# Optimization experiments

Measured on AMD Instinct MI355X. Metric: run time of the kernel, lower is better.

The kernel has to match this reference:

```python
import jax, jax.numpy as jnp
from jax import lax
import numpy as np

B, T, C, H = 2048, 1024, 9, 36  # batch, seq_len, input_size, hidden_size


def setup_inputs() -> dict:
    key = jax.random.key(0)
    ks = jax.random.split(key, 4)
    x = jax.random.normal(ks[0], (B, T, C), dtype=jnp.float32)
    # torch GRU param shapes: weight_ih (3H, C), weight_hh (3H, H), biases (3H,)
    w_ih = jax.random.normal(ks[1], (3 * H, C), dtype=jnp.float32) * (1.0 / np.sqrt(C))
    w_hh = jax.random.normal(ks[2], (3 * H, H), dtype=jnp.float32) * (1.0 / np.sqrt(H))
    b_ih = jnp.zeros((3 * H,), dtype=jnp.float32)
    b_hh = jnp.zeros((3 * H,), dtype=jnp.float32)
    w_head = jax.random.normal(ks[3], (1, H), dtype=jnp.float32) * (1.0 / np.sqrt(H))
    b_head = jnp.zeros((1,), dtype=jnp.float32)
    return {"x": x, "w_ih": w_ih, "w_hh": w_hh, "b_ih": b_ih, "b_hh": b_hh,
            "w_head": w_head, "b_head": b_head}


def reference(x, w_ih, w_hh, b_ih, b_hh, w_head, b_head):
    """TinyGRUInt8.forward in fp32 (Quant/DeQuant stubs are identity).
    GRU (batch_first, torch gate order r,z,n), take last timestep, Linear head.
    """
    h = w_hh.shape[1]
    # Precompute input contribution to all gates for every timestep: (B,T,3H)
    gx = jnp.einsum('btc,gc->btg', x, w_ih) + b_ih
    gx = jnp.moveaxis(gx, 1, 0)  # (T,B,3H) for scan over time

    def step(h_prev, gxt):
        gh = h_prev @ w_hh.T + b_hh                      # (B,3H)
        r = jax.nn.sigmoid(gxt[:, :h] + gh[:, :h])
        z = jax.nn.sigmoid(gxt[:, h:2 * h] + gh[:, h:2 * h])
        n = jnp.tanh(gxt[:, 2 * h:] + r * gh[:, 2 * h:])
        h_new = (1.0 - z) * n + z * h_prev
        return h_new, None

    h0 = jnp.zeros((x.shape[0], h), dtype=x.dtype)
    h_last, _ = lax.scan(step, h0, gx)                   # last output == final hidden
    return h_last @ w_head.T + b_head                    # (B,1)
```

## Files before the change

kernel.cpp:

```cpp
#include <hip/hip_runtime.h>

typedef float     v2f __attribute__((ext_vector_type(2)));
typedef _Float16  v2h __attribute__((ext_vector_type(2)));
typedef unsigned int uint;

#define BB 2048
#define TT 1024
#define CC 9
#define HH 36
#define G3 108
#define CSTEPS 64
#define CF (CSTEPS * CC)
#define XP 12
#define NCH (TT / CSTEPS)

__device__ __forceinline__ void lds_fence() {
    asm volatile("" ::: "memory");
    __builtin_amdgcn_sched_barrier(0);
}

__device__ __forceinline__ void pinh(v2h& v) {
    uint t = __builtin_bit_cast(uint, v);
    asm volatile("" : "+v"(t));
    v = __builtin_bit_cast(v2h, t);
}
__device__ __forceinline__ void pin2f(v2f& v) {
    uint64_t t = __builtin_bit_cast(uint64_t, v);
    asm volatile("" : "+v"(t));
    v = __builtin_bit_cast(v2f, t);
}

__device__ __forceinline__ void gload4(const float* g, float* l) {
    __builtin_amdgcn_global_load_lds(
        (const __attribute__((address_space(1))) unsigned int*)g,
        (__attribute__((address_space(3))) unsigned int*)l,
        4, 0, 0);
}

__global__ __launch_bounds__(64)
__attribute__((amdgpu_waves_per_eu(2, 2)))
void gru_kernel(
    const float* __restrict__ x,
    const float* __restrict__ w_ih,
    const float* __restrict__ w_hh,
    const float* __restrict__ b_ih,
    const float* __restrict__ b_hh,
    const float* __restrict__ w_head,
    const float* __restrict__ b_head,
    float* __restrict__ out)
{
    const int b = blockIdx.x;
    const int l = threadIdx.x;

    __shared__ __align__(16) float    fstage[CF];
    __shared__ __align__(16) float    xpad[CSTEPS * XP];
    __shared__ __align__(16) float    pbuf[256];
    __shared__ __align__(16) _Float16 hbuf[40];

    const int i0 = (2 * l     < G3) ? 2 * l     : G3 - 1;
    const int i1 = (2 * l + 1 < G3) ? 2 * l + 1 : G3 - 1;

    v2h wh0[18], wh1[18];
    v2f wx0[4], wx1[4];
    float w80, w81;
    float bA0, bB0, bA1, bB1;
    {
        const float* p0 = w_hh + (size_t)i0 * HH;
        const float* p1 = w_hh + (size_t)i1 * HH;
#pragma unroll
        for (int k = 0; k < 18; ++k) {
            wh0[k] = (v2h){(_Float16)p0[2*k], (_Float16)p0[2*k+1]};
            wh1[k] = (v2h){(_Float16)p1[2*k], (_Float16)p1[2*k+1]};
        }
        const float* q0 = w_ih + (size_t)i0 * CC;
        const float* q1 = w_ih + (size_t)i1 * CC;
#pragma unroll
        for (int p = 0; p < 4; ++p) {
            wx0[p] = (v2f){q0[2*p], q0[2*p+1]};
            wx1[p] = (v2f){q1[2*p], q1[2*p+1]};
        }
        w80 = q0[8];
        w81 = q1[8];
        const bool n0 = i0 >= 2 * HH, n1 = i1 >= 2 * HH;
        bA0 = n0 ? b_ih[i0] : (b_ih[i0] + b_hh[i0]);
        bB0 = n0 ? b_hh[i0] : 0.f;
        bA1 = n1 ? b_ih[i1] : (b_ih[i1] + b_hh[i1]);
        bB1 = n1 ? b_hh[i1] : 0.f;
    }
#pragma unroll
    for (int k = 0; k < 18; ++k) { pinh(wh0[k]); pinh(wh1[k]); }
#pragma unroll
    for (int p = 0; p < 4; ++p) { pin2f(wx0[p]); pin2f(wx1[p]); }
    asm volatile("" : "+v"(w80), "+v"(w81));
    asm volatile("" : "+v"(bA0), "+v"(bB0), "+v"(bA1), "+v"(bB1));

    const float* xg = x + (size_t)b * (TT * CC);

#pragma unroll
    for (int k = 0; k < 9; ++k) gload4(xg + k * 64 + l, &fstage[k * 64]);

    v2h h2[18];
#pragma unroll
    for (int k = 0; k < 18; ++k) h2[k] = (v2h){(_Float16)0.f, (_Float16)0.f};
    float h_own = 0.f;

    for (int c = 0; c < NCH; ++c) {
        asm volatile("s_waitcnt vmcnt(0)" ::: "memory");
        __builtin_amdgcn_sched_barrier(0);

        {
            float xf[9];
#pragma unroll
            for (int q = 0; q < 9; ++q) xf[q] = fstage[l * 9 + q];
            *(float4*)&xpad[l * XP]     = (float4){xf[0], xf[1], xf[2], xf[3]};
            *(float4*)&xpad[l * XP + 4] = (float4){xf[4], xf[5], xf[6], xf[7]};
            xpad[l * XP + 8] = xf[8];
        }
        lds_fence();

        if (c + 1 < NCH) {
            const float* src = xg + (size_t)(c + 1) * CF;
#pragma unroll
            for (int k = 0; k < 9; ++k) gload4(src + k * 64 + l, &fstage[k * 64]);
        }

#pragma unroll 2
        for (int s = 0; s < CSTEPS; ++s) {
            float4 xa = *(const float4*)&xpad[s * XP];
            float4 xb = *(const float4*)&xpad[s * XP + 4];
            float  x8 = xpad[s * XP + 8];
            v2f X0 = (v2f){xa.x, xa.y};
            v2f X1 = (v2f){xa.z, xa.w};
            v2f X2 = (v2f){xb.x, xb.y};
            v2f X3 = (v2f){xb.z, xb.w};

            v2f a0 = (v2f){bA0, 0.f};
            v2f a1 = (v2f){bA1, 0.f};
            a0 = __builtin_elementwise_fma(wx0[0], X0, a0);
            a1 = __builtin_elementwise_fma(wx1[0], X0, a1);
            a0 = __builtin_elementwise_fma(wx0[1], X1, a0);
            a1 = __builtin_elementwise_fma(wx1[1], X1, a1);
            a0 = __builtin_elementwise_fma(wx0[2], X2, a0);
            a1 = __builtin_elementwise_fma(wx1[2], X2, a1);
            a0 = __builtin_elementwise_fma(wx0[3], X3, a0);
            a1 = __builtin_elementwise_fma(wx1[3], X3, a1);
            float ax0 = fmaf(w80, x8, a0.x + a0.y);
            float ax1 = fmaf(w81, x8, a1.x + a1.y);

            float ah0 = bB0, ah1 = bB1;
#pragma unroll
            for (int k = 0; k < 18; ++k) {
                ah0 = __builtin_amdgcn_fdot2(wh0[k], h2[k], ah0, false);
                ah1 = __builtin_amdgcn_fdot2(wh1[k], h2[k], ah1, false);
            }

            *(float4*)&pbuf[4 * l] = (float4){ax0, ah0, ax1, ah1};
            lds_fence();

            if (l < HH) {
                v2f rp = *(const v2f*)&pbuf[2 * l];
                v2f zp = *(const v2f*)&pbuf[2 * (HH + l)];
                v2f np = *(const v2f*)&pbuf[2 * (2 * HH + l)];
                float sr = rp.x + rp.y;
                float sz = zp.x + zp.y;
                float r = __builtin_amdgcn_rcpf(1.f + __expf(-sr));
                float z = __builtin_amdgcn_rcpf(1.f + __expf(-sz));
                float a = np.x + r * np.y;
                float n = 1.f - 2.f * __builtin_amdgcn_rcpf(__expf(2.f * a) + 1.f);
                h_own = z * (h_own - n) + n;
                hbuf[l] = (_Float16)h_own;
            }
            lds_fence();

#pragma unroll
            for (int q = 0; q < 4; ++q) {
                uint4 t4 = ((const uint4*)hbuf)[q];
                h2[4*q+0] = __builtin_bit_cast(v2h, t4.x);
                h2[4*q+1] = __builtin_bit_cast(v2h, t4.y);
                h2[4*q+2] = __builtin_bit_cast(v2h, t4.z);
                h2[4*q+3] = __builtin_bit_cast(v2h, t4.w);
            }
            {
                uint2 t2 = ((const uint2*)hbuf)[8];
                h2[16] = __builtin_bit_cast(v2h, t2.x);
                h2[17] = __builtin_bit_cast(v2h, t2.y);
            }
        }
    }

    float whead = (l < HH) ? w_head[l] : 0.f;
    float v = (l < HH) ? h_own * whead : 0.f;
#pragma unroll
    for (int off = 32; off; off >>= 1) v += __shfl_down(v, off);
    if (l == 0) out[b] = v + b_head[0];
}

extern "C" void kernel_launch(void* const* d_in, const int* in_sizes, int n_in,
                              void* d_out, int out_size, void* d_ws, size_t ws_size,
                              hipStream_t stream) {
    const float* x      = (const float*)d_in[0];
    const float* w_ih   = (const float*)d_in[1];
    const float* w_hh   = (const float*)d_in[2];
    const float* b_ih   = (const float*)d_in[3];
    const float* b_hh   = (const float*)d_in[4];
    const float* w_head = (const float*)d_in[5];
    const float* b_head = (const float*)d_in[6];
    float* out = (float*)d_out;

    gru_kernel<<<BB, 64, 0, stream>>>(x, w_ih, w_hh, b_ih, b_hh,
                                      w_head, b_head, out);
}
```

Before: 411.9 us.

## Hoist input projection out of recurrent loop into per-chunk LDS gate buffer

Splits each chunk into two phases. First the input-gate projections for all CSTEPS timesteps are computed and stored in an LDS buffer, and only then does the serial recurrence run. The recurrence now reads precomputed gates and splits the fdot2 chain into two accumulators to shorten the dependency chain. The x staging now uses a padded gather layout, which removes the xpad repack pass, and the chunk size is halved. This takes the input projection off the serial critical path. The cost is an extra LDS round trip per step and less overlap of the x prefetch with compute.

```diff
diff --git a/kernel.cpp b/kernel.cpp
--- a/kernel.cpp
+++ b/kernel.cpp
@@ -9,9 +9,10 @@
 #define CC 9
 #define HH 36
 #define G3 108
-#define CSTEPS 64
+#define CSTEPS 32
 #define CF (CSTEPS * CC)
-#define XP 12
+#define FS 12
+#define GXS 112
 #define NCH (TT / CSTEPS)
 
 __device__ __forceinline__ void lds_fence() {
@@ -23,11 +24,6 @@
     uint t = __builtin_bit_cast(uint, v);
     asm volatile("" : "+v"(t));
     v = __builtin_bit_cast(v2h, t);
-}
-__device__ __forceinline__ void pin2f(v2f& v) {
-    uint64_t t = __builtin_bit_cast(uint64_t, v);
-    asm volatile("" : "+v"(t));
-    v = __builtin_bit_cast(v2f, t);
 }
 
 __device__ __forceinline__ void gload4(const float* g, float* l) {
@@ -52,18 +48,16 @@
     const int b = blockIdx.x;
     const int l = threadIdx.x;
 
-    __shared__ __align__(16) float    fstage[CF];
-    __shared__ __align__(16) float    xpad[CSTEPS * XP];
-    __shared__ __align__(16) float    pbuf[256];
+    __shared__ __align__(16) float    fstage[CSTEPS * FS];
+    __shared__ __align__(16) float    gxbuf[CSTEPS * GXS];
+    __shared__ __align__(16) float    ahbuf[128];
     __shared__ __align__(16) _Float16 hbuf[40];
 
     const int i0 = (2 * l     < G3) ? 2 * l     : G3 - 1;
     const int i1 = (2 * l + 1 < G3) ? 2 * l + 1 : G3 - 1;
 
     v2h wh0[18], wh1[18];
-    v2f wx0[4], wx1[4];
-    float w80, w81;
-    float bA0, bB0, bA1, bB1;
+    float bB0, bB1;
     {
         const float* p0 = w_hh + (size_t)i0 * HH;
         const float* p1 = w_hh + (size_t)i1 * HH;
@@ -72,6 +66,17 @@
             wh0[k] = (v2h){(_Float16)p0[2*k], (_Float16)p0[2*k+1]};
             wh1[k] = (v2h){(_Float16)p1[2*k], (_Float16)p1[2*k+1]};
         }
+        const bool n0 = i0 >= 2 * HH, n1 = i1 >= 2 * HH;
+        bB0 = n0 ? b_hh[i0] : 0.f;
+        bB1 = n1 ? b_hh[i1] : 0.f;
+    }
+#pragma unroll
+    for (int k = 0; k < 18; ++k) { pinh(wh0[k]); pinh(wh1[k]); }
+    asm volatile("" : "+v"(bB0), "+v"(bB1));
+
+    v2f wx0[4], wx1[4];
+    float w80, w81, bA0, bA1;
+    {
         const float* q0 = w_ih + (size_t)i0 * CC;
         const float* q1 = w_ih + (size_t)i1 * CC;
 #pragma unroll
@@ -83,21 +88,22 @@
         w81 = q1[8];
         const bool n0 = i0 >= 2 * HH, n1 = i1 >= 2 * HH;
         bA0 = n0 ? b_ih[i0] : (b_ih[i0] + b_hh[i0]);
-        bB0 = n0 ? b_hh[i0] : 0.f;
         bA1 = n1 ? b_ih[i1] : (b_ih[i1] + b_hh[i1]);
-        bB1 = n1 ? b_hh[i1] : 0.f;
-    }
-#pragma unroll
-    for (int k = 0; k < 18; ++k) { pinh(wh0[k]); pinh(wh1[k]); }
-#pragma unroll
-    for (int p = 0; p < 4; ++p) { pin2f(wx0[p]); pin2f(wx1[p]); }
-    asm volatile("" : "+v"(w80), "+v"(w81));
-    asm volatile("" : "+v"(bA0), "+v"(bB0), "+v"(bA1), "+v"(bB1));
+    }
+
+    int offk[6];
+#pragma unroll
+    for (int k = 0; k < 6; ++k) {
+        int idx = k * 64 + l;
+        int s   = idx / 12;
+        int q   = idx - 12 * s;
+        offk[k] = s * 9 + (q < 9 ? q : 8);
+    }
 
     const float* xg = x + (size_t)b * (TT * CC);
 
 #pragma unroll
-    for (int k = 0; k < 9; ++k) gload4(xg + k * 64 + l, &fstage[k * 64]);
+    for (int k = 0; k < 6; ++k) gload4(xg + offk[k], &fstage[k * 64]);
 
     v2h h2[18];
 #pragma unroll
@@ -108,32 +114,14 @@
         asm volatile("s_waitcnt vmcnt(0)" ::: "memory");
         __builtin_amdgcn_sched_barrier(0);
 
-        {
-            float xf[9];
-#pragma unroll
-            for (int q = 0; q < 9; ++q) xf[q] = fstage[l * 9 + q];
-            *(float4*)&xpad[l * XP]     = (float4){xf[0], xf[1], xf[2], xf[3]};
-            *(float4*)&xpad[l * XP + 4] = (float4){xf[4], xf[5], xf[6], xf[7]};
-            xpad[l * XP + 8] = xf[8];
-        }
-        lds_fence();
-
-        if (c + 1 < NCH) {
-            const float* src = xg + (size_t)(c + 1) * CF;
-#pragma unroll
-            for (int k = 0; k < 9; ++k) gload4(src + k * 64 + l, &fstage[k * 64]);
-        }
-
-#pragma unroll 2
         for (int s = 0; s < CSTEPS; ++s) {
-            float4 xa = *(const float4*)&xpad[s * XP];
-            float4 xb = *(const float4*)&xpad[s * XP + 4];
-            float  x8 = xpad[s * XP + 8];
+            float4 xa = *(const float4*)&fstage[s * FS];
+            float4 xc = *(const float4*)&fstage[s * FS + 4];
+            float  x8 = fstage[s * FS + 8];
             v2f X0 = (v2f){xa.x, xa.y};
             v2f X1 = (v2f){xa.z, xa.w};
-            v2f X2 = (v2f){xb.x, xb.y};
-            v2f X3 = (v2f){xb.z, xb.w};
-
+            v2f X2 = (v2f){xc.x, xc.y};
+            v2f X3 = (v2f){xc.z, xc.w};
             v2f a0 = (v2f){bA0, 0.f};
             v2f a1 = (v2f){bA1, 0.f};
             a0 = __builtin_elementwise_fma(wx0[0], X0, a0);
@@ -146,26 +134,43 @@
             a1 = __builtin_elementwise_fma(wx1[3], X3, a1);
             float ax0 = fmaf(w80, x8, a0.x + a0.y);
             float ax1 = fmaf(w81, x8, a1.x + a1.y);
-
-            float ah0 = bB0, ah1 = bB1;
-#pragma unroll
-            for (int k = 0; k < 18; ++k) {
-                ah0 = __builtin_amdgcn_fdot2(wh0[k], h2[k], ah0, false);
-                ah1 = __builtin_amdgcn_fdot2(wh1[k], h2[k], ah1, false);
-            }
-
-            *(float4*)&pbuf[4 * l] = (float4){ax0, ah0, ax1, ah1};
+            if (l < 54) *(v2f*)&gxbuf[s * GXS + 2 * l] = (v2f){ax0, ax1};
+        }
+        lds_fence();
+
+        if (c + 1 < NCH) {
+            const float* src = xg + (size_t)(c + 1) * CF;
+#pragma unroll
+            for (int k = 0; k < 6; ++k) gload4(src + offk[k], &fstage[k * 64]);
+        }
+
+        for (int s = 0; s < CSTEPS; ++s) {
+            float a0a = bB0, a1a = bB1, a0b = 0.f, a1b = 0.f;
+#pragma unroll
+            for (int k = 0; k < 9; ++k) {
+                a0a = __builtin_amdgcn_fdot2(wh0[k],     h2[k],     a0a, false);
+                a1a = __builtin_amdgcn_fdot2(wh1[k],     h2[k],     a1a, false);
+                a0b = __builtin_amdgcn_fdot2(wh0[k + 9], h2[k + 9], a0b, false);
+                a1b = __builtin_amdgcn_fdot2(wh1[k + 9], h2[k + 9], a1b, false);
+            }
+            float ah0 = a0a + a0b;
+            float ah1 = a1a + a1b;
+
+            *(v2f*)&ahbuf[2 * l] = (v2f){ah0, ah1};
             lds_fence();
 
             if (l < HH) {
-                v2f rp = *(const v2f*)&pbuf[2 * l];
-                v2f zp = *(const v2f*)&pbuf[2 * (HH + l)];
-                v2f np = *(const v2f*)&pbuf[2 * (2 * HH + l)];
-                float sr = rp.x + rp.y;
-                float sz = zp.x + zp.y;
+                float gxr = gxbuf[s * GXS + l];
+                float gxz = gxbuf[s * GXS + HH + l];
+                float gxn = gxbuf[s * GXS + 2 * HH + l];
+                float ahr = ahbuf[l];
+                float ahz = ahbuf[HH + l];
+                float ahn = ahbuf[2 * HH + l];
+                float sr = gxr + ahr;
+                float sz = gxz + ahz;
                 float r = __builtin_amdgcn_rcpf(1.f + __expf(-sr));
                 float z = __builtin_amdgcn_rcpf(1.f + __expf(-sz));
-                float a = np.x + r * np.y;
+                float a = gxn + r * ahn;
                 float n = 1.f - 2.f * __builtin_amdgcn_rcpf(__expf(2.f * a) + 1.f);
                 h_own = z * (h_own - n) + n;
                 hbuf[l] = (_Float16)h_own;
```

After: 412.7 us. About the same (+0.2%).
